# Performance work log

Hardware: AMD Instinct MI355X
Metric: run time of the kernel (lower is better)

Reference implementation:

```python
import jax, jax.numpy as jnp
import numpy as np

THRESH = 0.5
LENS = 0.5
DECAY = 0.5
CFG_FC = [256, 256, 256]
IN_SIZE = 1
OUT_SIZE = 10
T = 784 // IN_SIZE  # stride == input_size


def make_mask(dim, c_min, c_max, min_dc, max_dc, phase_shift_max, T=784):
    mask = []
    dc_steps = np.linspace(min_dc, max_dc, dim)
    cycles = np.linspace(c_min, c_max, dim)
    phase_shifts = np.linspace(0, int(phase_shift_max * c_max), dim)
    for cycle, dc, ps in zip(cycles, dc_steps, phase_shifts):
        cycle = int(np.ceil(cycle))
        on_length = int(np.ceil(dc * cycle))
        off_length = cycle - on_length
        pattern = [1] * on_length + [0] * off_length
        ps = int(np.round(ps))
        pattern = pattern[-ps:] + pattern[:-ps] if ps > 0 else pattern
        full_pattern = pattern * (T // cycle) + pattern[: T % cycle]
        mask.append(full_pattern)
    return jnp.asarray(np.array(mask, dtype=np.float32))  # [dim, T]


MASK1 = make_mask(CFG_FC[0], 4, 8, 0.1, 0.9, 0.5, T)
MASK2 = make_mask(CFG_FC[1], 4, 8, 0.1, 0.9, 0.5, T)
MASK3 = make_mask(CFG_FC[2], 4, 8, 0.1, 0.9, 0.5, T)


def act_fun(x):
    return (x > THRESH).astype(x.dtype)


def mem_update(x, mem, spike, mask):
    # mask: [H] broadcast over batch
    pre_mem = mem
    new_mem = mem * DECAY * (1.0 - spike) + x
    mem = jnp.where(mask == 0, pre_mem, new_mem)
    spike = act_fun(mem) * mask
    return mem, spike


def setup_inputs() -> dict:
    key = jax.random.key(0)
    ks = jax.random.split(key, 14)
    def lin(k, out_d, in_d):
        s = 1.0 / np.sqrt(in_d)
        return jax.random.uniform(k, (out_d, in_d), jnp.float32, -s, s)
    def bia(k, out_d, in_d):
        s = 1.0 / np.sqrt(in_d)
        return jax.random.uniform(k, (out_d,), jnp.float32, -s, s)
    H1, H2, H3 = CFG_FC
    return {
        "x": jax.random.uniform(ks[0], (512, 784), jnp.float32),
        "w_i2h1": lin(ks[1], H1, IN_SIZE), "b_i2h1": bia(ks[2], H1, IN_SIZE),
        "w_h2h1": lin(ks[3], H1, H1), "b_h2h1": bia(ks[4], H1, H1),
        "w_i2h2": lin(ks[5], H2, H1), "b_i2h2": bia(ks[6], H2, H1),
        "w_h2h2": lin(ks[7], H2, H2), "b_h2h2": bia(ks[8], H2, H2),
        "w_i2h3": lin(ks[9], H3, H2), "b_i2h3": bia(ks[10], H3, H2),
        "w_h2o3": lin(ks[11], OUT_SIZE, H3), "b_h2o3": bia(ks[12], OUT_SIZE, H3),
    }


def _build_x_seq(x):
    # replicate the torch slicing: start = step*stride, clamp to last window
    D = x.shape[1]
    starts = np.arange(T) * IN_SIZE
    starts = np.where(starts < T - IN_SIZE, starts, D - IN_SIZE)
    idx = starts[:, None] + np.arange(IN_SIZE)  # [T, in]
    x_seq = x[:, idx]                            # [N, T, in]
    return jnp.transpose(x_seq, (1, 0, 2))       # [T, N, in]


def reference(x, w_i2h1, b_i2h1, w_h2h1, b_h2h1, w_i2h2, b_i2h2,
              w_h2h2, b_h2h2, w_i2h3, b_i2h3, w_h2o3, b_h2o3):
    N = x.shape[0]
    H1, H2, H3 = CFG_FC
    x_seq = _build_x_seq(x)                       # [T, N, in]
    m1 = MASK1.T                                  # [T, H1]
    m2 = MASK2.T
    m3 = MASK3.T

    init = (jnp.zeros((N, H1)), jnp.zeros((N, H1)),
            jnp.zeros((N, H2)), jnp.zeros((N, H2)),
            jnp.zeros((N, H3)), jnp.zeros((N, H3)),
            jnp.zeros((N, OUT_SIZE)))

    def step(carry, inp):
        mem1, spk1, mem2, spk2, mem3, spk3, out_sum = carry
        xt, mk1, mk2, mk3 = inp
        h1 = xt @ w_i2h1.T + b_i2h1 + spk1 @ w_h2h1.T + b_h2h1
        mem1, spk1 = mem_update(h1, mem1, spk1, mk1)
        h2 = spk1 @ w_i2h2.T + b_i2h2 + spk2 @ w_h2h2.T + b_h2h2
        mem2, spk2 = mem_update(h2, mem2, spk2, mk2)
        h3 = spk2 @ w_i2h3.T + b_i2h3
        mem3, spk3 = mem_update(h3, mem3, spk3, mk3)
        out = spk3 @ w_h2o3.T + b_h2o3
        return (mem1, spk1, mem2, spk2, mem3, spk3, out_sum + out), None

    (final, _) = jax.lax.scan(step, init, (x_seq, m1, m2, m3))
    out_sum = final[-1]
    return out_sum / T
```

## Files before the change

### kernel.cpp

```cpp
#include <hip/hip_runtime.h>
#include <stdint.h>

#define T_STEPS 784
#define H 256
#define NBLK 512
#define NTHR 256

typedef unsigned long long u64;

__device__ __forceinline__ void mask_params(int j, int& c, int& on, int& ps) {
    const double stepc = (8.0 - 4.0) / 255.0;
    const double stepd = (0.9 - 0.1) / 255.0;
    const double stepp = 4.0 / 255.0;
    double cyc = (j == 255) ? 8.0 : __dadd_rn(__dmul_rn((double)j, stepc), 4.0);
    c = (int)ceil(cyc);
    double dc  = (j == 255) ? 0.9 : __dadd_rn(__dmul_rn((double)j, stepd), 0.1);
    on = (int)ceil(__dmul_rn(dc, (double)c));
    double psd = (j == 255) ? 4.0 : __dmul_rn((double)j, stepp);
    ps = (int)rint(psd);
}

__device__ __forceinline__ void acc_add(const float4& w, float4& a) {
    a.x += w.x; a.y += w.y; a.z += w.z; a.w += w.w;
}

__device__ __forceinline__ void consume64(const char* __restrict__ base, u64 m,
                                          int l16, float4& acc) {
    int n = __popcll(m);
    while (n >= 8) {
        int k0=__builtin_ctzll(m); m&=m-1; int k1=__builtin_ctzll(m); m&=m-1;
        int k2=__builtin_ctzll(m); m&=m-1; int k3=__builtin_ctzll(m); m&=m-1;
        int k4=__builtin_ctzll(m); m&=m-1; int k5=__builtin_ctzll(m); m&=m-1;
        int k6=__builtin_ctzll(m); m&=m-1; int k7=__builtin_ctzll(m); m&=m-1;
        float4 w0 = *(const float4*)(base + (k0<<10) + l16);
        float4 w1 = *(const float4*)(base + (k1<<10) + l16);
        float4 w2 = *(const float4*)(base + (k2<<10) + l16);
        float4 w3 = *(const float4*)(base + (k3<<10) + l16);
        float4 w4 = *(const float4*)(base + (k4<<10) + l16);
        float4 w5 = *(const float4*)(base + (k5<<10) + l16);
        float4 w6 = *(const float4*)(base + (k6<<10) + l16);
        float4 w7 = *(const float4*)(base + (k7<<10) + l16);
        acc_add(w0, acc); acc_add(w1, acc); acc_add(w2, acc); acc_add(w3, acc);
        acc_add(w4, acc); acc_add(w5, acc); acc_add(w6, acc); acc_add(w7, acc);
        n -= 8;
    }
    if (n & 4) {
        int k0=__builtin_ctzll(m); m&=m-1; int k1=__builtin_ctzll(m); m&=m-1;
        int k2=__builtin_ctzll(m); m&=m-1; int k3=__builtin_ctzll(m); m&=m-1;
        float4 w0 = *(const float4*)(base + (k0<<10) + l16);
        float4 w1 = *(const float4*)(base + (k1<<10) + l16);
        float4 w2 = *(const float4*)(base + (k2<<10) + l16);
        float4 w3 = *(const float4*)(base + (k3<<10) + l16);
        acc_add(w0, acc); acc_add(w1, acc); acc_add(w2, acc); acc_add(w3, acc);
    }
    if (n & 2) {
        int k0=__builtin_ctzll(m); m&=m-1; int k1=__builtin_ctzll(m); m&=m-1;
        float4 w0 = *(const float4*)(base + (k0<<10) + l16);
        float4 w1 = *(const float4*)(base + (k1<<10) + l16);
        acc_add(w0, acc); acc_add(w1, acc);
    }
    if (n & 1) {
        int k0 = __builtin_ctzll(m);
        float4 w0 = *(const float4*)(base + (k0<<10) + l16);
        acc_add(w0, acc);
    }
}

__device__ __forceinline__ void upd(float& mem, float& sp, float h, int mbit) {
    float nm = fmaf(mem * 0.5f, (1.0f - sp), h);
    mem = mbit ? nm : mem;
    sp  = (mbit && (mem > 0.5f)) ? 1.0f : 0.0f;
}

__global__ __launch_bounds__(256)
void prep_transpose(const float* __restrict__ w1, const float* __restrict__ w2a,
                    const float* __restrict__ w2b, const float* __restrict__ w3,
                    float* __restrict__ ws)
{
    __shared__ float tile[64][65];
    const int bid = blockIdx.x;
    const int m  = bid >> 4;
    const int kt = (bid >> 2) & 3;
    const int jt = bid & 3;
    const float* src = (m == 0) ? w1 : (m == 1) ? w2a : (m == 2) ? w2b : w3;
    float* dst = ws + (size_t)m * H * H;
    const int tid = threadIdx.x;
    const int c = tid & 63, r4 = tid >> 6;
    #pragma unroll
    for (int rr = 0; rr < 16; rr++) {
        int r = r4 * 16 + rr;
        tile[r][c] = src[(size_t)(jt * 64 + r) * H + kt * 64 + c];
    }
    __syncthreads();
    #pragma unroll
    for (int rr = 0; rr < 16; rr++) {
        int r = r4 * 16 + rr;
        dst[(size_t)(kt * 64 + r) * H + jt * 64 + c] = tile[c][r];
    }
}

__global__ __launch_bounds__(NTHR, 2)
void srnn_kernel(const float* __restrict__ x,
                 const float* __restrict__ w_i2h1, const float* __restrict__ b_i2h1,
                 const float* __restrict__ b_h2h1,
                 const float* __restrict__ b_i2h2, const float* __restrict__ b_h2h2,
                 const float* __restrict__ b_i2h3,
                 const float* __restrict__ w_h2o3, const float* __restrict__ b_h2o3,
                 const float* __restrict__ ws,
                 float* __restrict__ out)
{
    const int tid  = threadIdx.x;
    const int lane = tid & 63;
    const int w    = tid >> 6;
    const int j    = tid;
    const int l16  = lane * 16;
    const int s    = blockIdx.x;

    const char* wt1  = (const char*)ws + (0 << 18) + (w << 16);
    const char* wt2a = (const char*)ws + (1 << 18) + (w << 16);
    const char* wt2b = (const char*)ws + (2 << 18) + (w << 16);
    const char* wt3  = (const char*)ws + (3 << 18) + (w << 16);

    __shared__ float xls[T_STEPS];
    __shared__ float pexA[2][4][H];
    __shared__ float pexB[2][4][H];
    __shared__ float pexC[2][4][H];
    __shared__ float wred[4][10];

    for (int i = tid; i < T_STEPS; i += NTHR)
        xls[i] = x[(size_t)s * T_STEPS + i];

    int mc, mon, mps;
    mask_params(j, mc, mon, mps);
    int ph = (mc - (mps % mc)) % mc;

    const float bs1 = b_i2h1[j] + b_h2h1[j];
    const float bs2 = b_i2h2[j] + b_h2h2[j];
    const float bs3 = b_i2h3[j];
    const float wi1 = w_i2h1[j];

    float mem1 = 0.f, mem2 = 0.f, mem3 = 0.f;
    float sp1 = 0.f, sp2 = 0.f, sp3 = 0.f;
    u64 bal1 = 0ull, bal2 = 0ull;
    int mb_d1 = 0, mb_d2 = 0;
    float cnt = 0.f;

    __syncthreads();

    for (int sl = 0; sl < T_STEPS + 2; sl++) {
        const int par  = sl & 1;
        const int mbit = (ph < mon) ? 1 : 0;
        const bool runL1 = (sl < T_STEPS);
        const bool runL2 = (sl >= 1) && (sl <= T_STEPS);
        const bool runL3 = (sl >= 2);

        if (runL1) {
            float4 a = {0.f, 0.f, 0.f, 0.f};
            consume64(wt1, bal1, l16, a);
            ((float4*)pexA[par][w])[lane] = a;
        }
        if (runL2) {
            float4 a = {0.f, 0.f, 0.f, 0.f};
            consume64(wt2b, bal2, l16, a);
            consume64(wt2a, bal1, l16, a);
            ((float4*)pexB[par][w])[lane] = a;
        }
        if (runL3) {
            float4 a = {0.f, 0.f, 0.f, 0.f};
            consume64(wt3, bal2, l16, a);
            ((float4*)pexC[par][w])[lane] = a;
        }
        __syncthreads();

        u64 nb1 = bal1, nb2 = bal2;
        if (runL1) {
            float hs = (pexA[par][0][j] + pexA[par][1][j])
                     + (pexA[par][2][j] + pexA[par][3][j]);
            float h1 = hs + fmaf(xls[sl], wi1, bs1);
            upd(mem1, sp1, h1, mbit);
            nb1 = __ballot(sp1 != 0.0f);
        }
        if (runL2) {
            float hs = (pexB[par][0][j] + pexB[par][1][j])
                     + (pexB[par][2][j] + pexB[par][3][j]);
            upd(mem2, sp2, hs + bs2, mb_d1);
            nb2 = __ballot(sp2 != 0.0f);
        }
        if (runL3) {
            float hs = (pexC[par][0][j] + pexC[par][1][j])
                     + (pexC[par][2][j] + pexC[par][3][j]);
            upd(mem3, sp3, hs + bs3, mb_d2);
            cnt += sp3;
        }
        bal1 = nb1; bal2 = nb2;
        mb_d2 = mb_d1; mb_d1 = mbit;
        ph++; if (ph == mc) ph = 0;
    }

    #pragma unroll
    for (int i = 0; i < 10; i++) {
        float v = cnt * w_h2o3[i * H + j];
        for (int off = 32; off; off >>= 1) v += __shfl_down(v, off, 64);
        if (lane == 0) wred[w][i] = v;
    }
    __syncthreads();
    if (tid < 10) {
        float sum = wred[0][tid] + wred[1][tid] + wred[2][tid] + wred[3][tid];
        out[(size_t)s * 10 + tid] = sum / 784.0f + b_h2o3[tid];
    }
}

extern "C" void kernel_launch(void* const* d_in, const int* in_sizes, int n_in,
                              void* d_out, int out_size, void* d_ws, size_t ws_size,
                              hipStream_t stream) {
    (void)in_sizes; (void)n_in; (void)ws_size; (void)out_size;
    const float* x      = (const float*)d_in[0];
    const float* w_i2h1 = (const float*)d_in[1];
    const float* b_i2h1 = (const float*)d_in[2];
    const float* w_h2h1 = (const float*)d_in[3];
    const float* b_h2h1 = (const float*)d_in[4];
    const float* w_i2h2 = (const float*)d_in[5];
    const float* b_i2h2 = (const float*)d_in[6];
    const float* w_h2h2 = (const float*)d_in[7];
    const float* b_h2h2 = (const float*)d_in[8];
    const float* w_i2h3 = (const float*)d_in[9];
    const float* b_i2h3 = (const float*)d_in[10];
    const float* w_h2o3 = (const float*)d_in[11];
    const float* b_h2o3 = (const float*)d_in[12];
    float* ws = (float*)d_ws;

    prep_transpose<<<64, 256, 0, stream>>>(w_h2h1, w_i2h2, w_h2h2, w_i2h3, ws);
    srnn_kernel<<<NBLK, NTHR, 0, stream>>>(x,
        w_i2h1, b_i2h1, b_h2h1,
        b_i2h2, b_h2h2, b_i2h3,
        w_h2o3, b_h2o3, ws,
        (float*)d_out);
}
```

Baseline: 2.098 ms.

## Software-pipeline sparse weight gathers, sharing spike masks across layer pairs

```diff
diff --git a/kernel.cpp b/kernel.cpp
--- a/kernel.cpp
+++ b/kernel.cpp
@@ -22,48 +22,6 @@
 
 __device__ __forceinline__ void acc_add(const float4& w, float4& a) {
     a.x += w.x; a.y += w.y; a.z += w.z; a.w += w.w;
-}
-
-__device__ __forceinline__ void consume64(const char* __restrict__ base, u64 m,
-                                          int l16, float4& acc) {
-    int n = __popcll(m);
-    while (n >= 8) {
-        int k0=__builtin_ctzll(m); m&=m-1; int k1=__builtin_ctzll(m); m&=m-1;
-        int k2=__builtin_ctzll(m); m&=m-1; int k3=__builtin_ctzll(m); m&=m-1;
-        int k4=__builtin_ctzll(m); m&=m-1; int k5=__builtin_ctzll(m); m&=m-1;
-        int k6=__builtin_ctzll(m); m&=m-1; int k7=__builtin_ctzll(m); m&=m-1;
-        float4 w0 = *(const float4*)(base + (k0<<10) + l16);
-        float4 w1 = *(const float4*)(base + (k1<<10) + l16);
-        float4 w2 = *(const float4*)(base + (k2<<10) + l16);
-        float4 w3 = *(const float4*)(base + (k3<<10) + l16);
-        float4 w4 = *(const float4*)(base + (k4<<10) + l16);
-        float4 w5 = *(const float4*)(base + (k5<<10) + l16);
-        float4 w6 = *(const float4*)(base + (k6<<10) + l16);
-        float4 w7 = *(const float4*)(base + (k7<<10) + l16);
-        acc_add(w0, acc); acc_add(w1, acc); acc_add(w2, acc); acc_add(w3, acc);
-        acc_add(w4, acc); acc_add(w5, acc); acc_add(w6, acc); acc_add(w7, acc);
-        n -= 8;
-    }
-    if (n & 4) {
-        int k0=__builtin_ctzll(m); m&=m-1; int k1=__builtin_ctzll(m); m&=m-1;
-        int k2=__builtin_ctzll(m); m&=m-1; int k3=__builtin_ctzll(m); m&=m-1;
-        float4 w0 = *(const float4*)(base + (k0<<10) + l16);
-        float4 w1 = *(const float4*)(base + (k1<<10) + l16);
-        float4 w2 = *(const float4*)(base + (k2<<10) + l16);
-        float4 w3 = *(const float4*)(base + (k3<<10) + l16);
-        acc_add(w0, acc); acc_add(w1, acc); acc_add(w2, acc); acc_add(w3, acc);
-    }
-    if (n & 2) {
-        int k0=__builtin_ctzll(m); m&=m-1; int k1=__builtin_ctzll(m); m&=m-1;
-        float4 w0 = *(const float4*)(base + (k0<<10) + l16);
-        float4 w1 = *(const float4*)(base + (k1<<10) + l16);
-        acc_add(w0, acc); acc_add(w1, acc);
-    }
-    if (n & 1) {
-        int k0 = __builtin_ctzll(m);
-        float4 w0 = *(const float4*)(base + (k0<<10) + l16);
-        acc_add(w0, acc);
-    }
 }
 
 __device__ __forceinline__ void upd(float& mem, float& sp, float h, int mbit) {
@@ -99,6 +57,36 @@
     }
 }
 
+struct B4 {
+    float4 p0, p1, p2, p3;
+    float4 q0, q1, q2, q3;
+    int c;
+};
+
+#define ISS(Bt, m, n, bX, bY)                                              \
+    {   int c_ = (n < 4) ? n : 4;                                          \
+        Bt.c = c_;                                                         \
+        if (c_ > 0) { int k_=(int)__builtin_ctzll(m); m&=m-1;              \
+            Bt.p0 = *(const float4*)(bX + (k_<<10) + l16);                 \
+            Bt.q0 = *(const float4*)(bY + (k_<<10) + l16); }               \
+        if (c_ > 1) { int k_=(int)__builtin_ctzll(m); m&=m-1;              \
+            Bt.p1 = *(const float4*)(bX + (k_<<10) + l16);                 \
+            Bt.q1 = *(const float4*)(bY + (k_<<10) + l16); }               \
+        if (c_ > 2) { int k_=(int)__builtin_ctzll(m); m&=m-1;              \
+            Bt.p2 = *(const float4*)(bX + (k_<<10) + l16);                 \
+            Bt.q2 = *(const float4*)(bY + (k_<<10) + l16); }               \
+        if (c_ > 3) { int k_=(int)__builtin_ctzll(m); m&=m-1;              \
+            Bt.p3 = *(const float4*)(bX + (k_<<10) + l16);                 \
+            Bt.q3 = *(const float4*)(bY + (k_<<10) + l16); }               \
+        n -= c_; }
+
+#define RED(Bt, aX, aY)                                                    \
+    {   if (Bt.c > 0) { acc_add(Bt.p0, aX); acc_add(Bt.q0, aY); }          \
+        if (Bt.c > 1) { acc_add(Bt.p1, aX); acc_add(Bt.q1, aY); }          \
+        if (Bt.c > 2) { acc_add(Bt.p2, aX); acc_add(Bt.q2, aY); }          \
+        if (Bt.c > 3) { acc_add(Bt.p3, aX); acc_add(Bt.q3, aY); }          \
+        Bt.c = 0; }
+
 __global__ __launch_bounds__(NTHR, 2)
 void srnn_kernel(const float* __restrict__ x,
                  const float* __restrict__ w_i2h1, const float* __restrict__ b_i2h1,
@@ -154,37 +142,44 @@
         const bool runL2 = (sl >= 1) && (sl <= T_STEPS);
         const bool runL3 = (sl >= 2);
 
-        if (runL1) {
-            float4 a = {0.f, 0.f, 0.f, 0.f};
-            consume64(wt1, bal1, l16, a);
-            ((float4*)pexA[par][w])[lane] = a;
-        }
-        if (runL2) {
-            float4 a = {0.f, 0.f, 0.f, 0.f};
-            consume64(wt2b, bal2, l16, a);
-            consume64(wt2a, bal1, l16, a);
-            ((float4*)pexB[par][w])[lane] = a;
-        }
-        if (runL3) {
-            float4 a = {0.f, 0.f, 0.f, 0.f};
-            consume64(wt3, bal2, l16, a);
-            ((float4*)pexC[par][w])[lane] = a;
-        }
+        float4 accA = {0.f,0.f,0.f,0.f}, accB = {0.f,0.f,0.f,0.f}, accC = {0.f,0.f,0.f,0.f};
+        {
+            u64 m1 = bal1, m2 = bal2;
+            int n1 = __popcll(m1), n2 = __popcll(m2);
+            B4 A0, A1, C0, C1;
+            A0.c = 0; A1.c = 0; C0.c = 0; C1.c = 0;
+            ISS(A0, m1, n1, wt1, wt2a);
+            ISS(C0, m2, n2, wt2b, wt3);
+            while (n1 > 0 || n2 > 0) {
+                ISS(A1, m1, n1, wt1, wt2a);
+                RED(A0, accA, accB);
+                ISS(C1, m2, n2, wt2b, wt3);
+                RED(C0, accB, accC);
+                ISS(A0, m1, n1, wt1, wt2a);
+                RED(A1, accA, accB);
+                ISS(C0, m2, n2, wt2b, wt3);
+                RED(C1, accB, accC);
+            }
+            RED(A0, accA, accB); RED(A1, accA, accB);
+            RED(C0, accB, accC); RED(C1, accB, accC);
+        }
+        if (runL1) ((float4*)pexA[par][w])[lane] = accA;
+        if (runL2) ((float4*)pexB[par][w])[lane] = accB;
+        if (runL3) ((float4*)pexC[par][w])[lane] = accC;
         __syncthreads();
 
-        u64 nb1 = bal1, nb2 = bal2;
         if (runL1) {
             float hs = (pexA[par][0][j] + pexA[par][1][j])
                      + (pexA[par][2][j] + pexA[par][3][j]);
             float h1 = hs + fmaf(xls[sl], wi1, bs1);
             upd(mem1, sp1, h1, mbit);
-            nb1 = __ballot(sp1 != 0.0f);
+            bal1 = __ballot(sp1 != 0.0f);
         }
         if (runL2) {
             float hs = (pexB[par][0][j] + pexB[par][1][j])
                      + (pexB[par][2][j] + pexB[par][3][j]);
             upd(mem2, sp2, hs + bs2, mb_d1);
-            nb2 = __ballot(sp2 != 0.0f);
+            bal2 = __ballot(sp2 != 0.0f);
         }
         if (runL3) {
             float hs = (pexC[par][0][j] + pexC[par][1][j])
@@ -192,7 +187,6 @@
             upd(mem3, sp3, hs + bs3, mb_d2);
             cnt += sp3;
         }
-        bal1 = nb1; bal2 = nb2;
         mb_d2 = mb_d1; mb_d1 = mbit;
         ph++; if (ph == mc) ph = 0;
     }
```

After: 2.927 ms. +39.5%, slower.
